# Kernel tuning notes

Hardware: AMD Instinct MI355X
Metric: run time of the kernel (lower is better)

The kernel has to match this reference:

```python
import jax, jax.numpy as jnp
import numpy as np

BLOCK_SPLIT = (4, 4, 4)
GRID = 256
N_BLOCK = 64
BX = GRID // 4  # 64, per-block grid resolution along each axis
N_PTS = 4_194_304


def setup_inputs() -> dict:
    key = jax.random.key(0)
    k1, k2 = jax.random.split(key)
    aabb = jnp.array([[-1.5, -1.5, -1.5], [1.5, 1.5, 1.5]], dtype=jnp.float32)
    # points roughly inside the aabb
    xyz_sampled = jax.random.uniform(k1, (N_PTS, 3), dtype=jnp.float32) * 3.0 - 1.5
    alpha_volume = jax.random.uniform(k2, (GRID, GRID, GRID), dtype=jnp.float32)
    # per-block domains (as kilonerf global_to_local expects): block AABBs
    idx = np.stack(np.meshgrid(np.arange(4), np.arange(4), np.arange(4), indexing='ij'), -1).reshape(-1, 3)
    voxel = np.array([3.0 / 4.0] * 3)
    dmin = (-1.5 + idx * voxel).astype(np.float32)
    dmax = (dmin + voxel).astype(np.float32)
    return {"xyz_sampled": xyz_sampled, "aabb": aabb, "alpha_volume": alpha_volume,
            "domain_min": jnp.asarray(dmin), "domain_max": jnp.asarray(dmax)}


def _sample_alpha(xyz, aabb, alpha_volume, dmin, dmax):
    bs = jnp.asarray(BLOCK_SPLIT, jnp.float32)
    voxel = (aabb[1] - aabb[0]) / bs                      # per-block world size
    idx3 = jnp.floor((xyz - aabb[0]) / voxel).astype(jnp.int32)
    idx3 = jnp.clip(idx3, 0, jnp.array(BLOCK_SPLIT, jnp.int32) - 1)  # edge clamp (matches loop)
    strides = jnp.array([BLOCK_SPLIT[2] * BLOCK_SPLIT[1], BLOCK_SPLIT[2], 1], jnp.int32)
    bid = (idx3 * strides).sum(-1)                        # [N] block id in [0, 64)

    order = jnp.argsort(bid)                              # jax sort is stable; matches bucket-by-block order
    bid_s = bid[order]
    pts = xyz[order]

    # global_to_local (kilonerf): map into per-block [-1,1]^3
    local = 2.0 * (pts - dmin[bid_s]) / (dmax[bid_s] - dmin[bid_s]) - 1.0  # [N,3] (gx,gy,gz)

    # torch .view(64,1,64,64,64) is a raw contiguous reinterpretation -> plain reshape
    vols = alpha_volume.reshape(N_BLOCK, BX, BX, BX)      # [B, D, H, W]
    D = H = W = BX
    # grid_sample convention: grid x -> W axis, y -> H axis, z -> D axis; align_corners=True
    fx = (local[:, 0] + 1.0) * 0.5 * (W - 1)
    fy = (local[:, 1] + 1.0) * 0.5 * (H - 1)
    fz = (local[:, 2] + 1.0) * 0.5 * (D - 1)
    x0 = jnp.floor(fx); y0 = jnp.floor(fy); z0 = jnp.floor(fz)
    wx = fx - x0; wy = fy - y0; wz = fz - z0
    x0i = x0.astype(jnp.int32); y0i = y0.astype(jnp.int32); z0i = z0.astype(jnp.int32)

    def fetch(zi, yi, xi):
        # zeros padding for out-of-range corners (grid_sample padding_mode='zeros')
        inb = (zi >= 0) & (zi < D) & (yi >= 0) & (yi < H) & (xi >= 0) & (xi < W)
        v = vols[bid_s, jnp.clip(zi, 0, D - 1), jnp.clip(yi, 0, H - 1), jnp.clip(xi, 0, W - 1)]
        return jnp.where(inb, v, 0.0)

    out = jnp.zeros_like(fx)
    for dz, wz_ in ((0, 1.0 - wz), (1, wz)):
        for dy, wy_ in ((0, 1.0 - wy), (1, wy)):
            for dx, wx_ in ((0, 1.0 - wx), (1, wx)):
                out = out + wz_ * wy_ * wx_ * fetch(z0i + dz, y0i + dy, x0i + dx)
    return out  # [N] alpha values in block-sorted order


def reference(xyz_sampled, aabb, alpha_volume, domain_min, domain_max):
    return _sample_alpha(xyz_sampled, aabb, alpha_volume, domain_min, domain_max)
```

## Files before the change

kernel.cpp:

```cpp
#include <hip/hip_runtime.h>

#define NB     64
#define NF     4096
#define TILE   16384
#define HBLK   1024
#define DBLK   1024
#define FBLK   512
#define GBLK   256
#define SBLK   256
#define FB_TILE 4096

__device__ __forceinline__ int compute_bid(float px, float py, float pz,
                                           float a0x, float a0y, float a0z,
                                           float vx, float vy, float vz) {
    int ix = (int)floorf((px - a0x) / vx);
    int iy = (int)floorf((py - a0y) / vy);
    int iz = (int)floorf((pz - a0z) / vz);
    ix = min(max(ix, 0), 3);
    iy = min(max(iy, 0), 3);
    iz = min(max(iz, 0), 3);
    return ix * 16 + iy * 4 + iz;
}

__device__ __forceinline__ void quant_point(float px, float py, float pz,
        float a0x, float a0y, float a0z, float vx, float vy, float vz,
        const float* s_dn, const float* s_sc,
        int& b, int& qx, int& qy, int& qz, int& key) {
    b = compute_bid(px, py, pz, a0x, a0y, a0z, vx, vy, vz);
    float fx = (px - s_dn[3 * b])     * s_sc[3 * b];
    float fy = (py - s_dn[3 * b + 1]) * s_sc[3 * b + 1];
    float fz = (pz - s_dn[3 * b + 2]) * s_sc[3 * b + 2];
    qx = min(max(__float2int_rn(fx * 256.0f), 0), 16128);
    qy = min(max(__float2int_rn(fy * 256.0f), 0), 16128);
    qz = min(max(__float2int_rn(fz * 256.0f), 0), 16128);
    key = (b << 6) | ((qz >> 12) << 4) | ((qy >> 12) << 2) | (qx >> 12);
}

__global__ void __launch_bounds__(HBLK) hist_kernel(
        const float* __restrict__ xyz, const float* __restrict__ aabb,
        const float* __restrict__ dmin, const float* __restrict__ dmax,
        int* __restrict__ hist64, int* __restrict__ tot4096, int N, int T) {
    __shared__ int   sh[NF];
    __shared__ float s_dn[192], s_sc[192];
    const int tid = threadIdx.x, g = blockIdx.x;
    for (int l = tid; l < NF; l += HBLK) sh[l] = 0;
    if (tid < 192) { s_dn[tid] = dmin[tid]; s_sc[tid] = 63.0f / (dmax[tid] - dmin[tid]); }
    const float a0x = aabb[0], a0y = aabb[1], a0z = aabb[2];
    const float vx = (aabb[3] - a0x) * 0.25f;
    const float vy = (aabb[4] - a0y) * 0.25f;
    const float vz = (aabb[5] - a0z) * 0.25f;
    __syncthreads();
    for (int c = 0; c < TILE / (HBLK * 4); ++c) {
        int p0 = g * TILE + c * (HBLK * 4) + tid * 4;
        int b, qx, qy, qz, k;
        if (p0 + 3 < N) {
            const float4* v4 = (const float4*)(xyz + (size_t)p0 * 3);
            float4 f0 = v4[0], f1 = v4[1], f2 = v4[2];
            quant_point(f0.x, f0.y, f0.z, a0x, a0y, a0z, vx, vy, vz, s_dn, s_sc, b, qx, qy, qz, k);
            atomicAdd(&sh[k], 1);
            quant_point(f0.w, f1.x, f1.y, a0x, a0y, a0z, vx, vy, vz, s_dn, s_sc, b, qx, qy, qz, k);
            atomicAdd(&sh[k], 1);
            quant_point(f1.z, f1.w, f2.x, a0x, a0y, a0z, vx, vy, vz, s_dn, s_sc, b, qx, qy, qz, k);
            atomicAdd(&sh[k], 1);
            quant_point(f2.y, f2.z, f2.w, a0x, a0y, a0z, vx, vy, vz, s_dn, s_sc, b, qx, qy, qz, k);
            atomicAdd(&sh[k], 1);
        } else {
            for (int t = 0; t < 4; ++t) {
                int i = p0 + t;
                if (i < N) {
                    quant_point(xyz[3 * i], xyz[3 * i + 1], xyz[3 * i + 2],
                                a0x, a0y, a0z, vx, vy, vz, s_dn, s_sc, b, qx, qy, qz, k);
                    atomicAdd(&sh[k], 1);
                }
            }
        }
    }
    __syncthreads();
    for (int l = tid; l < NF; l += HBLK) {
        int c = sh[l];
        if (c) atomicAdd(&tot4096[l], c);
    }
    if (tid < NB) {
        int s = 0;
        #pragma unroll
        for (int j = 0; j < 64; ++j) s += sh[tid * 64 + j];
        hist64[tid * T + g] = s;
    }
}

__global__ void scans_kernel(int* __restrict__ hist64, int* __restrict__ tot64,
                             const int* __restrict__ tot4096,
                             int* __restrict__ foff, int* __restrict__ fcnt, int G) {
    __shared__ int sh[SBLK];
    const int t = threadIdx.x;
    if (blockIdx.x < NB) {
        const int b = blockIdx.x;
        const int L = (G + SBLK - 1) / SBLK;
        const int lo = t * L;
        const int n = min(L, max(0, G - lo));
        const int base = b * G + lo;
        int s = 0;
        for (int k = 0; k < n; ++k) s += hist64[base + k];
        sh[t] = s;
        __syncthreads();
        for (int off = 1; off < SBLK; off <<= 1) {
            int v = (t >= off) ? sh[t - off] : 0;
            __syncthreads();
            sh[t] += v;
            __syncthreads();
        }
        int excl = (t == 0) ? 0 : sh[t - 1];
        for (int k = 0; k < n; ++k) {
            int v = hist64[base + k];
            hist64[base + k] = excl;
            excl += v;
        }
        if (t == SBLK - 1) tot64[b] = sh[SBLK - 1];
    } else {
        const int L = NF / SBLK;
        int loc[16];
        int s = 0;
        #pragma unroll
        for (int j = 0; j < L; ++j) { loc[j] = tot4096[t * L + j]; s += loc[j]; }
        sh[t] = s;
        __syncthreads();
        for (int o = 1; o < SBLK; o <<= 1) {
            int v = (t >= o) ? sh[t - o] : 0;
            __syncthreads();
            sh[t] += v;
            __syncthreads();
        }
        int run = (t == 0) ? 0 : sh[t - 1];
        #pragma unroll
        for (int j = 0; j < L; ++j) {
            foff[t * L + j] = run;
            fcnt[t * L + j] = run;
            run += loc[j];
        }
        if (t == SBLK - 1) foff[NF] = run;
    }
}

__global__ void __launch_bounds__(DBLK) scatterC_kernel(
        const float* __restrict__ xyz, const float* __restrict__ aabb,
        const float* __restrict__ dmin, const float* __restrict__ dmax,
        const int* __restrict__ hist64, const int* __restrict__ tot64,
        unsigned long long* __restrict__ payloadC, int N, int T) {
    __shared__ int   s_wh[16][NB];
    __shared__ int   s_cnt0[NB];
    __shared__ int   s_off[NB];
    __shared__ float s_dn[192], s_sc[192];
    const int tid = threadIdx.x, g = blockIdx.x;
    const int lane = tid & 63, wv = tid >> 6;
    if (tid < NB) s_off[tid] = tot64[tid];
    if (tid < 192) { s_dn[tid] = dmin[tid]; s_sc[tid] = 63.0f / (dmax[tid] - dmin[tid]); }
    ((int*)s_wh)[tid] = 0;
    const float a0x = aabb[0], a0y = aabb[1], a0z = aabb[2];
    const float vx = (aabb[3] - a0x) * 0.25f;
    const float vy = (aabb[4] - a0y) * 0.25f;
    const float vz = (aabb[5] - a0z) * 0.25f;
    __syncthreads();
    for (int o = 1; o < NB; o <<= 1) {
        int v = (tid < NB && tid >= o) ? s_off[tid - o] : 0;
        __syncthreads();
        if (tid < NB) s_off[tid] += v;
        __syncthreads();
    }
    if (tid < NB) s_cnt0[tid] = hist64[tid * T + g] + (tid ? s_off[tid - 1] : 0);

    const unsigned long long lt = (1ull << lane) - 1ull;
    const int base_i = g * TILE + wv * 1024;
    unsigned long long cache[16];
    #pragma unroll
    for (int r = 0; r < 16; ++r) {
        int i = base_i + r * 64 + lane;
        bool valid = (i < N);
        int b = 0, qx = 0, qy = 0, qz = 0, key;
        if (valid) {
            quant_point(xyz[3 * i], xyz[3 * i + 1], xyz[3 * i + 2],
                        a0x, a0y, a0z, vx, vy, vz, s_dn, s_sc, b, qx, qy, qz, key);
        }
        unsigned long long m = __ballot(valid);
        #pragma unroll
        for (int q = 0; q < 6; ++q) {
            unsigned long long bal = __ballot((b >> q) & 1);
            m &= ((b >> q) & 1) ? bal : ~bal;
        }
        int rank = __popcll(m & lt);
        int run = valid ? s_wh[wv][b] : 0;
        if (valid && rank == 0) s_wh[wv][b] = run + __popcll(m);
        int localpos = run + rank;
        cache[r] = (unsigned long long)(unsigned)qx
                 | ((unsigned long long)(unsigned)qy << 14)
                 | ((unsigned long long)(unsigned)qz << 28)
                 | ((unsigned long long)(unsigned)b  << 42)
                 | ((unsigned long long)(unsigned)localpos << 48);
    }
    __syncthreads();
    for (int o = 1; o < 16; o <<= 1) {
        int v = (wv >= o) ? s_wh[wv - o][lane] : 0;
        __syncthreads();
        s_wh[wv][lane] += v;
        __syncthreads();
    }
    #pragma unroll
    for (int r = 0; r < 16; ++r) {
        int i = base_i + r * 64 + lane;
        if (i < N) {
            unsigned long long cc = cache[r];
            int b = (int)((cc >> 42) & 63);
            int localpos = (int)((cc >> 48) & 1023);
            int pos = s_cnt0[b] + (wv ? s_wh[wv - 1][b] : 0) + localpos;
            payloadC[pos] = cc & ((1ull << 48) - 1);
        }
    }
}

__global__ void __launch_bounds__(FBLK) scatterF_kernel(
        const unsigned long long* __restrict__ payloadC,
        int* __restrict__ fcnt,
        unsigned long long* __restrict__ payloadF, int N) {
    __shared__ int s_fb[NF];
    const int tid = threadIdx.x, t2 = blockIdx.x;
    for (int l = tid; l < NF; l += FBLK) s_fb[l] = 0;
    __syncthreads();
    const int lo = t2 * TILE;
    const int n = min(TILE, N - lo);
    for (int j = tid; j < n; j += FBLK) {
        unsigned long long p = payloadC[lo + j];
        int qx = (int)(p & 16383), qy = (int)((p >> 14) & 16383);
        int qz = (int)((p >> 28) & 16383), b = (int)((p >> 42) & 63);
        int key = (b << 6) | ((qz >> 12) << 4) | ((qy >> 12) << 2) | (qx >> 12);
        atomicAdd(&s_fb[key], 1);
    }
    __syncthreads();
    for (int l = tid; l < NF; l += FBLK) {
        int c = s_fb[l];
        s_fb[l] = c ? atomicAdd(&fcnt[l], c) : 0;
    }
    __syncthreads();
    for (int j = tid; j < n; j += FBLK) {
        unsigned long long p = payloadC[lo + j];
        int qx = (int)(p & 16383), qy = (int)((p >> 14) & 16383);
        int qz = (int)((p >> 28) & 16383), b = (int)((p >> 42) & 63);
        int key = (b << 6) | ((qz >> 12) << 4) | ((qy >> 12) << 2) | (qx >> 12);
        int fpos = atomicAdd(&s_fb[key], 1);
        payloadF[fpos] = (p & ((1ull << 42) - 1))
                       | ((unsigned long long)(unsigned)(lo + j) << 42);
    }
}

__global__ void __launch_bounds__(GBLK) gather_kernel(
        const float* __restrict__ vol,
        const unsigned long long* __restrict__ payloadF,
        const int* __restrict__ foff, float* __restrict__ out) {
    __shared__ float sv[17 * 17 * 17];
    const int tid = threadIdx.x;
    const int nb = gridDim.x, d = blockIdx.x;
    const int k = (nb % 8 == 0) ? (d % 8) * (nb / 8) + (d / 8) : d;
    const int b = k >> 6;
    const int bz = ((k >> 4) & 3) * 16, by = ((k >> 2) & 3) * 16, bx = (k & 3) * 16;
    const float* vb = vol + ((size_t)b << 18);
    for (int l = tid; l < 17 * 17 * 17; l += GBLK) {
        int z = l / 289, r = l - z * 289, y = r / 17, x = r - y * 17;
        int gz = bz + z, gy = by + y, gx = bx + x;
        sv[l] = (gz < 64 && gy < 64 && gx < 64)
                    ? vb[(gz << 12) + (gy << 6) + gx] : 0.0f;
    }
    __syncthreads();
    const int lo = foff[k];
    const int n = foff[k + 1] - lo;
    for (int j = tid; j < n; j += GBLK) {
        unsigned long long p = payloadF[lo + j];
        int qx = (int)(p & 16383), qy = (int)((p >> 14) & 16383);
        int qz = (int)((p >> 28) & 16383);
        int pos = (int)(p >> 42);
        float wx = (qx & 255) * (1.0f / 256.0f);
        float wy = (qy & 255) * (1.0f / 256.0f);
        float wz = (qz & 255) * (1.0f / 256.0f);
        int lx = (qx >> 8) - bx, ly = (qy >> 8) - by, lz = (qz >> 8) - bz;
        int base = lz * 289 + ly * 17 + lx;
        float v000 = sv[base],       v001 = sv[base + 1];
        float v010 = sv[base + 17],  v011 = sv[base + 18];
        float v100 = sv[base + 289], v101 = sv[base + 290];
        float v110 = sv[base + 306], v111 = sv[base + 307];
        float c00 = v000 + wx * (v001 - v000);
        float c01 = v010 + wx * (v011 - v010);
        float c10 = v100 + wx * (v101 - v100);
        float c11 = v110 + wx * (v111 - v110);
        float c0 = c00 + wy * (c01 - c00);
        float c1 = c10 + wy * (c11 - c10);
        out[pos] = c0 + wz * (c1 - c0);
    }
}

__global__ void fb_hist_kernel(const float* __restrict__ xyz,
                               const float* __restrict__ aabb,
                               int* __restrict__ hist, int N, int G) {
    __shared__ int s_h[NB];
    const int tid = threadIdx.x, g = blockIdx.x;
    if (tid < NB) s_h[tid] = 0;
    __syncthreads();
    const float a0x = aabb[0], a0y = aabb[1], a0z = aabb[2];
    const float vx = (aabb[3] - a0x) * 0.25f;
    const float vy = (aabb[4] - a0y) * 0.25f;
    const float vz = (aabb[5] - a0z) * 0.25f;
    for (int c = 0; c < FB_TILE / 256; ++c) {
        int i = g * FB_TILE + c * 256 + tid;
        if (i < N)
            atomicAdd(&s_h[compute_bid(xyz[3 * i], xyz[3 * i + 1], xyz[3 * i + 2],
                                       a0x, a0y, a0z, vx, vy, vz)], 1);
    }
    __syncthreads();
    if (tid < NB) hist[tid * G + g] = s_h[tid];
}

__global__ void fb_scan_kernel(int* __restrict__ hist, int* __restrict__ tot, int G) {
    __shared__ int sh[SBLK];
    const int b = blockIdx.x, t = threadIdx.x;
    const int L = (G + SBLK - 1) / SBLK;
    const int lo = t * L;
    const int n = min(L, max(0, G - lo));
    const int base = b * G + lo;
    int s = 0;
    for (int k = 0; k < n; ++k) s += hist[base + k];
    sh[t] = s;
    __syncthreads();
    for (int off = 1; off < SBLK; off <<= 1) {
        int v = (t >= off) ? sh[t - off] : 0;
        __syncthreads();
        sh[t] += v;
        __syncthreads();
    }
    int excl = (t == 0) ? 0 : sh[t - 1];
    for (int k = 0; k < n; ++k) {
        int v = hist[base + k];
        hist[base + k] = excl;
        excl += v;
    }
    if (t == SBLK - 1) tot[b] = sh[SBLK - 1];
}

__global__ void fb_scatter_kernel(const float* __restrict__ xyz,
                                  const float* __restrict__ aabb,
                                  const float* __restrict__ dmin,
                                  const float* __restrict__ dmax,
                                  const float* __restrict__ vol,
                                  const int* __restrict__ hist,
                                  const int* __restrict__ tot64,
                                  float* __restrict__ out, int N, int G) {
    __shared__ int   s_cnt[NB], s_off[NB];
    __shared__ int   s_whist[4][NB];
    __shared__ float s_dn[192], s_sc[192];
    const int tid = threadIdx.x, g = blockIdx.x;
    if (tid < NB) s_off[tid] = tot64[tid];
    if (tid < 192) { s_dn[tid] = dmin[tid]; s_sc[tid] = 63.0f / (dmax[tid] - dmin[tid]); }
    __syncthreads();
    for (int o = 1; o < NB; o <<= 1) {
        int v = (tid < NB && tid >= o) ? s_off[tid - o] : 0;
        __syncthreads();
        if (tid < NB) s_off[tid] += v;
        __syncthreads();
    }
    if (tid < NB) s_cnt[tid] = hist[tid * G + g] + (tid ? s_off[tid - 1] : 0);
    const float a0x = aabb[0], a0y = aabb[1], a0z = aabb[2];
    const float vx = (aabb[3] - a0x) * 0.25f;
    const float vy = (aabb[4] - a0y) * 0.25f;
    const float vz = (aabb[5] - a0z) * 0.25f;
    __syncthreads();
    const int lane = tid & 63, wv = tid >> 6;
    const unsigned long long lt = (1ull << lane) - 1ull;
    for (int c = 0; c < FB_TILE / 256; ++c) {
        int i = g * FB_TILE + c * 256 + tid;
        bool valid = (i < N);
        int b = 0;
        float alpha = 0.0f;
        if (valid) {
            float px = xyz[3 * i], py = xyz[3 * i + 1], pz = xyz[3 * i + 2];
            b = compute_bid(px, py, pz, a0x, a0y, a0z, vx, vy, vz);
            float fx = (px - s_dn[3 * b])     * s_sc[3 * b];
            float fy = (py - s_dn[3 * b + 1]) * s_sc[3 * b + 1];
            float fz = (pz - s_dn[3 * b + 2]) * s_sc[3 * b + 2];
            float x0f = floorf(fx), y0f = floorf(fy), z0f = floorf(fz);
            float wx = fx - x0f, wy = fy - y0f, wz = fz - z0f;
            int x0 = (int)x0f, y0 = (int)y0f, z0 = (int)z0f;
            const float* vb = vol + ((size_t)b << 18);
            auto F = [&](int zi, int yi, int xi) -> float {
                if ((unsigned)zi >= 64u || (unsigned)yi >= 64u || (unsigned)xi >= 64u)
                    return 0.0f;
                return vb[(zi << 12) + (yi << 6) + xi];
            };
            float s = 0.0f;
            s += (1.0f - wz) * (1.0f - wy) * (1.0f - wx) * F(z0,     y0,     x0);
            s += (1.0f - wz) * (1.0f - wy) * wx          * F(z0,     y0,     x0 + 1);
            s += (1.0f - wz) * wy          * (1.0f - wx) * F(z0,     y0 + 1, x0);
            s += (1.0f - wz) * wy          * wx          * F(z0,     y0 + 1, x0 + 1);
            s += wz          * (1.0f - wy) * (1.0f - wx) * F(z0 + 1, y0,     x0);
            s += wz          * (1.0f - wy) * wx          * F(z0 + 1, y0,     x0 + 1);
            s += wz          * wy          * (1.0f - wx) * F(z0 + 1, y0 + 1, x0);
            s += wz          * wy          * wx          * F(z0 + 1, y0 + 1, x0 + 1);
            alpha = s;
        }
        ((int*)s_whist)[tid] = 0;
        __syncthreads();
        unsigned long long m = __ballot(valid);
        #pragma unroll
        for (int q = 0; q < 6; ++q) {
            unsigned long long bal = __ballot((b >> q) & 1);
            m &= ((b >> q) & 1) ? bal : ~bal;
        }
        int rank = __popcll(m & lt);
        if (valid && rank == 0) s_whist[wv][b] = __popcll(m);
        __syncthreads();
        if (valid) {
            int pos = s_cnt[b] + rank;
            for (int w2 = 0; w2 < wv; ++w2) pos += s_whist[w2][b];
            out[pos] = alpha;
        }
        __syncthreads();
        if (tid < NB)
            s_cnt[tid] += s_whist[0][tid] + s_whist[1][tid] +
                          s_whist[2][tid] + s_whist[3][tid];
        __syncthreads();
    }
}

extern "C" void kernel_launch(void* const* d_in, const int* in_sizes, int n_in,
                              void* d_out, int out_size, void* d_ws, size_t ws_size,
                              hipStream_t stream) {
    const float* xyz  = (const float*)d_in[0];
    const float* aabb = (const float*)d_in[1];
    const float* vol  = (const float*)d_in[2];
    const float* dmin = (const float*)d_in[3];
    const float* dmax = (const float*)d_in[4];
    float* out = (float*)d_out;
    const int N = in_sizes[0] / 3;
    const int T = (N + TILE - 1) / TILE;

    auto align = [](size_t x) { return (x + 255) & ~(size_t)255; };
    char* ws = (char*)d_ws;
    size_t o = 0;
    unsigned long long* payloadC = (unsigned long long*)(ws + o); o += align((size_t)N * 8);
    unsigned long long* payloadF = (unsigned long long*)(ws + o); o += align((size_t)N * 8);
    int* hist64  = (int*)(ws + o); o += align((size_t)NB * T * 4);
    int* tot64   = (int*)(ws + o); o += 256;
    int* tot4096 = (int*)(ws + o); o += align((size_t)NF * 4);
    int* foff    = (int*)(ws + o); o += align((size_t)(NF + 1) * 4);
    int* fcnt    = (int*)(ws + o); o += align((size_t)NF * 4);
    const bool fine = (N <= (1 << 22)) && (ws_size >= o);

    if (fine) {
        hipMemsetAsync(tot4096, 0, NF * 4, stream);
        hist_kernel<<<T, HBLK, 0, stream>>>(xyz, aabb, dmin, dmax,
                                            hist64, tot4096, N, T);
        scans_kernel<<<NB + 1, SBLK, 0, stream>>>(hist64, tot64, tot4096,
                                                  foff, fcnt, T);
        scatterC_kernel<<<T, DBLK, 0, stream>>>(xyz, aabb, dmin, dmax,
                                                hist64, tot64, payloadC, N, T);
        scatterF_kernel<<<T, FBLK, 0, stream>>>(payloadC, fcnt, payloadF, N);
        gather_kernel<<<NF, GBLK, 0, stream>>>(vol, payloadF, foff, out);
    } else {
        const int Gf = (N + FB_TILE - 1) / FB_TILE;
        int* h = (int*)ws;
        int* t = (int*)(ws + align((size_t)NB * Gf * 4));
        fb_hist_kernel<<<Gf, 256, 0, stream>>>(xyz, aabb, h, N, Gf);
        fb_scan_kernel<<<NB, SBLK, 0, stream>>>(h, t, Gf);
        fb_scatter_kernel<<<Gf, 256, 0, stream>>>(xyz, aabb, dmin, dmax, vol,
                                                  h, t, out, N, Gf);
    }
}
```

Measured before the change: 280.4 us.

## Stage bucketed payloads in LDS for coalesced global scatter

The coarse scatter kernel now computes each element's position within the tile's block-sorted order, writes the payloads into a 64 KB shared-memory staging buffer in two halves, and then writes them out to global memory in sorted order. Each bucket's run becomes a contiguous segment, so global writes are mostly coalesced instead of scattered per element. The cost is extra LDS traffic, more barriers and a large shared allocation that may reduce occupancy.

```diff
diff --git a/kernel.cpp b/kernel.cpp
--- a/kernel.cpp
+++ b/kernel.cpp
@@ -9,6 +9,7 @@
 #define GBLK   256
 #define SBLK   256
 #define FB_TILE 4096
+#define STAGE_HALF 8192
 
 __device__ __forceinline__ int compute_bid(float px, float py, float pz,
                                            float a0x, float a0y, float a0z,
@@ -146,9 +147,12 @@
         const float* __restrict__ dmin, const float* __restrict__ dmax,
         const int* __restrict__ hist64, const int* __restrict__ tot64,
         unsigned long long* __restrict__ payloadC, int N, int T) {
+    __shared__ unsigned long long stage[STAGE_HALF];
     __shared__ int   s_wh[16][NB];
     __shared__ int   s_cnt0[NB];
     __shared__ int   s_off[NB];
+    __shared__ int   s_start[NB];
+    __shared__ int   s_gb[NB];
     __shared__ float s_dn[192], s_sc[192];
     const int tid = threadIdx.x, g = blockIdx.x;
     const int lane = tid & 63, wv = tid >> 6;
@@ -203,6 +207,20 @@
         s_wh[wv][lane] += v;
         __syncthreads();
     }
+    if (wv == 0) {
+        int v = s_wh[15][lane];
+        int incl = v;
+        #pragma unroll
+        for (int o = 1; o < 64; o <<= 1) {
+            int u = __shfl_up(incl, o);
+            if (lane >= o) incl += u;
+        }
+        int excl = incl - v;
+        s_start[lane] = excl;
+        s_gb[lane] = s_cnt0[lane] - excl;
+    }
+    __syncthreads();
+    const int n = min(TILE, N - g * TILE);
     #pragma unroll
     for (int r = 0; r < 16; ++r) {
         int i = base_i + r * 64 + lane;
@@ -210,9 +228,37 @@
             unsigned long long cc = cache[r];
             int b = (int)((cc >> 42) & 63);
             int localpos = (int)((cc >> 48) & 1023);
-            int pos = s_cnt0[b] + (wv ? s_wh[wv - 1][b] : 0) + localpos;
-            payloadC[pos] = cc & ((1ull << 48) - 1);
-        }
+            int lidx = s_start[b] + (wv ? s_wh[wv - 1][b] : 0) + localpos;
+            unsigned long long p48 = cc & ((1ull << 48) - 1);
+            if (lidx < STAGE_HALF) stage[lidx] = p48;
+            cache[r] = p48 | ((unsigned long long)(unsigned)lidx << 48);
+        }
+    }
+    __syncthreads();
+    {
+        int nA = min(n, STAGE_HALF);
+        for (int j = tid; j < nA; j += DBLK) {
+            unsigned long long p = stage[j];
+            int b = (int)((p >> 42) & 63);
+            payloadC[s_gb[b] + j] = p;
+        }
+    }
+    __syncthreads();
+    #pragma unroll
+    for (int r = 0; r < 16; ++r) {
+        int i = base_i + r * 64 + lane;
+        if (i < N) {
+            unsigned long long cc = cache[r];
+            int lidx = (int)(cc >> 48);
+            if (lidx >= STAGE_HALF)
+                stage[lidx - STAGE_HALF] = cc & ((1ull << 48) - 1);
+        }
+    }
+    __syncthreads();
+    for (int j = STAGE_HALF + tid; j < n; j += DBLK) {
+        unsigned long long p = stage[j - STAGE_HALF];
+        int b = (int)((p >> 42) & 63);
+        payloadC[s_gb[b] + j] = p;
     }
 }
 
```

After: 256.6 us. 1.09x faster.

## Fuse coarse and fine scatter kernels and load gather tiles directly into LDS

Applied to the files above, without the earlier changes.

Merges the block-level scatter and the fine-bucket scatter into one kernel. Each point's fine bucket slot is now computed from the register cache, so the intermediate coarse payload buffer is never written and read back, and one launch is removed. The gather kernel now fills its 17^3 shared-memory tile with global_load_lds direct-to-LDS loads, using a zeroed dummy address for out-of-range cells. The fused kernel needs 16KB more LDS per 1024-thread block, and it does more global atomics per tile because there are fewer points per fine bucket per block.

```diff
diff --git a/kernel.cpp b/kernel.cpp
--- a/kernel.cpp
+++ b/kernel.cpp
@@ -5,10 +5,12 @@
 #define TILE   16384
 #define HBLK   1024
 #define DBLK   1024
-#define FBLK   512
 #define GBLK   256
 #define SBLK   256
 #define FB_TILE 4096
+
+#define GLOBAL_AS __attribute__((address_space(1)))
+#define LDS_AS    __attribute__((address_space(3)))
 
 __device__ __forceinline__ int compute_bid(float px, float py, float pz,
                                            float a0x, float a0y, float a0z,
@@ -141,11 +143,13 @@
     }
 }
 
-__global__ void __launch_bounds__(DBLK) scatterC_kernel(
+__global__ void __launch_bounds__(DBLK) scatterCF_kernel(
         const float* __restrict__ xyz, const float* __restrict__ aabb,
         const float* __restrict__ dmin, const float* __restrict__ dmax,
         const int* __restrict__ hist64, const int* __restrict__ tot64,
-        unsigned long long* __restrict__ payloadC, int N, int T) {
+        int* __restrict__ fcnt,
+        unsigned long long* __restrict__ payloadF, int N, int T) {
+    __shared__ int   s_fb[NF];
     __shared__ int   s_wh[16][NB];
     __shared__ int   s_cnt0[NB];
     __shared__ int   s_off[NB];
@@ -155,6 +159,7 @@
     if (tid < NB) s_off[tid] = tot64[tid];
     if (tid < 192) { s_dn[tid] = dmin[tid]; s_sc[tid] = 63.0f / (dmax[tid] - dmin[tid]); }
     ((int*)s_wh)[tid] = 0;
+    for (int l = tid; l < NF; l += DBLK) s_fb[l] = 0;
     const float a0x = aabb[0], a0y = aabb[1], a0z = aabb[2];
     const float vx = (aabb[3] - a0x) * 0.25f;
     const float vy = (aabb[4] - a0y) * 0.25f;
@@ -197,12 +202,29 @@
                  | ((unsigned long long)(unsigned)localpos << 48);
     }
     __syncthreads();
+    #pragma unroll
+    for (int r = 0; r < 16; ++r) {
+        int i = base_i + r * 64 + lane;
+        if (i < N) {
+            unsigned long long cc = cache[r];
+            int qx = (int)(cc & 16383), qy = (int)((cc >> 14) & 16383);
+            int qz = (int)((cc >> 28) & 16383), b = (int)((cc >> 42) & 63);
+            int key = (b << 6) | ((qz >> 12) << 4) | ((qy >> 12) << 2) | (qx >> 12);
+            atomicAdd(&s_fb[key], 1);
+        }
+    }
+    __syncthreads();
     for (int o = 1; o < 16; o <<= 1) {
         int v = (wv >= o) ? s_wh[wv - o][lane] : 0;
         __syncthreads();
         s_wh[wv][lane] += v;
         __syncthreads();
     }
+    for (int l = tid; l < NF; l += DBLK) {
+        int c = s_fb[l];
+        s_fb[l] = c ? atomicAdd(&fcnt[l], c) : 0;
+    }
+    __syncthreads();
     #pragma unroll
     for (int r = 0; r < 16; ++r) {
         int i = base_i + r * 64 + lane;
@@ -211,61 +233,37 @@
             int b = (int)((cc >> 42) & 63);
             int localpos = (int)((cc >> 48) & 1023);
             int pos = s_cnt0[b] + (wv ? s_wh[wv - 1][b] : 0) + localpos;
-            payloadC[pos] = cc & ((1ull << 48) - 1);
-        }
-    }
-}
-
-__global__ void __launch_bounds__(FBLK) scatterF_kernel(
-        const unsigned long long* __restrict__ payloadC,
-        int* __restrict__ fcnt,
-        unsigned long long* __restrict__ payloadF, int N) {
-    __shared__ int s_fb[NF];
-    const int tid = threadIdx.x, t2 = blockIdx.x;
-    for (int l = tid; l < NF; l += FBLK) s_fb[l] = 0;
-    __syncthreads();
-    const int lo = t2 * TILE;
-    const int n = min(TILE, N - lo);
-    for (int j = tid; j < n; j += FBLK) {
-        unsigned long long p = payloadC[lo + j];
-        int qx = (int)(p & 16383), qy = (int)((p >> 14) & 16383);
-        int qz = (int)((p >> 28) & 16383), b = (int)((p >> 42) & 63);
-        int key = (b << 6) | ((qz >> 12) << 4) | ((qy >> 12) << 2) | (qx >> 12);
-        atomicAdd(&s_fb[key], 1);
-    }
-    __syncthreads();
-    for (int l = tid; l < NF; l += FBLK) {
-        int c = s_fb[l];
-        s_fb[l] = c ? atomicAdd(&fcnt[l], c) : 0;
-    }
-    __syncthreads();
-    for (int j = tid; j < n; j += FBLK) {
-        unsigned long long p = payloadC[lo + j];
-        int qx = (int)(p & 16383), qy = (int)((p >> 14) & 16383);
-        int qz = (int)((p >> 28) & 16383), b = (int)((p >> 42) & 63);
-        int key = (b << 6) | ((qz >> 12) << 4) | ((qy >> 12) << 2) | (qx >> 12);
-        int fpos = atomicAdd(&s_fb[key], 1);
-        payloadF[fpos] = (p & ((1ull << 42) - 1))
-                       | ((unsigned long long)(unsigned)(lo + j) << 42);
+            int qx = (int)(cc & 16383), qy = (int)((cc >> 14) & 16383);
+            int qz = (int)((cc >> 28) & 16383);
+            int key = (b << 6) | ((qz >> 12) << 4) | ((qy >> 12) << 2) | (qx >> 12);
+            int fpos = atomicAdd(&s_fb[key], 1);
+            payloadF[fpos] = (cc & ((1ull << 42) - 1))
+                           | ((unsigned long long)(unsigned)pos << 42);
+        }
     }
 }
 
 __global__ void __launch_bounds__(GBLK) gather_kernel(
         const float* __restrict__ vol,
         const unsigned long long* __restrict__ payloadF,
-        const int* __restrict__ foff, float* __restrict__ out) {
-    __shared__ float sv[17 * 17 * 17];
+        const int* __restrict__ foff, const float* __restrict__ zf,
+        float* __restrict__ out) {
+    __shared__ float sv[77 * 64];
     const int tid = threadIdx.x;
+    const int lane = tid & 63, wv = tid >> 6;
     const int nb = gridDim.x, d = blockIdx.x;
     const int k = (nb % 8 == 0) ? (d % 8) * (nb / 8) + (d / 8) : d;
     const int b = k >> 6;
     const int bz = ((k >> 4) & 3) * 16, by = ((k >> 2) & 3) * 16, bx = (k & 3) * 16;
     const float* vb = vol + ((size_t)b << 18);
-    for (int l = tid; l < 17 * 17 * 17; l += GBLK) {
+    for (int m = wv; m < 77; m += GBLK / 64) {
+        int l = m * 64 + lane;
         int z = l / 289, r = l - z * 289, y = r / 17, x = r - y * 17;
         int gz = bz + z, gy = by + y, gx = bx + x;
-        sv[l] = (gz < 64 && gy < 64 && gx < 64)
-                    ? vb[(gz << 12) + (gy << 6) + gx] : 0.0f;
+        bool ok = (l < 17 * 17 * 17) && (gz < 64) && (gy < 64) && (gx < 64);
+        const float* src = ok ? (vb + ((gz << 12) + (gy << 6) + gx)) : zf;
+        __builtin_amdgcn_global_load_lds((const GLOBAL_AS void*)src,
+                                         (LDS_AS void*)(sv + m * 64), 4, 0, 0);
     }
     __syncthreads();
     const int lo = foff[k];
@@ -440,25 +438,27 @@
     auto align = [](size_t x) { return (x + 255) & ~(size_t)255; };
     char* ws = (char*)d_ws;
     size_t o = 0;
-    unsigned long long* payloadC = (unsigned long long*)(ws + o); o += align((size_t)N * 8);
     unsigned long long* payloadF = (unsigned long long*)(ws + o); o += align((size_t)N * 8);
     int* hist64  = (int*)(ws + o); o += align((size_t)NB * T * 4);
     int* tot64   = (int*)(ws + o); o += 256;
+    size_t zbase = o;
     int* tot4096 = (int*)(ws + o); o += align((size_t)NF * 4);
     int* foff    = (int*)(ws + o); o += align((size_t)(NF + 1) * 4);
     int* fcnt    = (int*)(ws + o); o += align((size_t)NF * 4);
+    float* zf    = (float*)(ws + o); o += 256;
+    size_t zlen = o - zbase;
     const bool fine = (N <= (1 << 22)) && (ws_size >= o);
 
     if (fine) {
-        hipMemsetAsync(tot4096, 0, NF * 4, stream);
+        hipMemsetAsync(ws + zbase, 0, zlen, stream);
         hist_kernel<<<T, HBLK, 0, stream>>>(xyz, aabb, dmin, dmax,
                                             hist64, tot4096, N, T);
         scans_kernel<<<NB + 1, SBLK, 0, stream>>>(hist64, tot64, tot4096,
                                                   foff, fcnt, T);
-        scatterC_kernel<<<T, DBLK, 0, stream>>>(xyz, aabb, dmin, dmax,
-                                                hist64, tot64, payloadC, N, T);
-        scatterF_kernel<<<T, FBLK, 0, stream>>>(payloadC, fcnt, payloadF, N);
-        gather_kernel<<<NF, GBLK, 0, stream>>>(vol, payloadF, foff, out);
+        scatterCF_kernel<<<T, DBLK, 0, stream>>>(xyz, aabb, dmin, dmax,
+                                                 hist64, tot64, fcnt,
+                                                 payloadF, N, T);
+        gather_kernel<<<NF, GBLK, 0, stream>>>(vol, payloadF, foff, zf, out);
     } else {
         const int Gf = (N + FB_TILE - 1) / FB_TILE;
         int* h = (int*)ws;
```

Measured after the change: 279.8 us. No clear change (-0.2%).
